# Kernel tuning notes

Measured on AMD Instinct MI355X. Metric: run time of the kernel, lower is better.

## Reference

```python
import jax, jax.numpy as jnp
import numpy as np

B, N, D = 512, 256, 128
N_LAYER, N_HEAD = 4, 1
VAR = 0.01
HEAD = 0  # head_choice in run_mode=0


def setup_inputs() -> dict:
    key = jax.random.key(0)
    k1, k2 = jax.random.split(key)
    Z = jax.random.normal(k1, (B, N + 1, D + 1), dtype=jnp.float32)
    # allparam ~ N(0, var): torch .normal_(0, var) uses var as stddev
    allparam = jax.random.normal(k2, (N_LAYER, N_HEAD, 2, D, D), dtype=jnp.float32) * VAR
    gamma = jnp.ones((N_LAYER, N_HEAD, 1, N + 1, D + 1), dtype=jnp.float32)
    return {"Z": Z, "allparam": allparam, "gamma": gamma}


def _pad_full(M, corner):
    # Embed d x d matrix in (d+1) x (d+1) with zeros; set bottom-right corner.
    d = M.shape[0]
    full = jnp.zeros((d + 1, d + 1), M.dtype).at[:d, :d].set(M)
    return full.at[d, d].set(corner)


def _attention(P, Q, Z):
    # Z: [B, N+1, d+1]
    n = Z.shape[1] - 1
    P_full = _pad_full(P, 1.0)   # P with 1 at [d, d]
    Q_full = _pad_full(Q, 0.0)
    Attn = jnp.einsum('bni,ij,bmj->bnm', Z, Q_full, Z)  # [B, N+1, N+1]
    key = jnp.einsum('ij,bnj->bni', P_full, Z)           # [B, N+1, d+1]
    # A = eye(N+1) with A[N, N] = 0  <=>  zero the last token's key row
    key = key.at[:, n, :].set(0.0)
    return jnp.einsum('bnm,bmi->bni', Attn, key) / n


def reference(Z, allparam, gamma):
    # run_mode=0, chosen head = HEAD
    # T_i = R_i + sum_{k<i} R_k * gamma_k ; Z <- Z + T_i
    acc = jnp.zeros_like(Z)  # running sum_{k<i} R_k * gamma_k
    for i in range(N_LAYER):
        P = allparam[i, HEAD, 0]
        Q = allparam[i, HEAD, 1]
        R = _attention(P, Q, Z)
        T = R + acc
        acc = acc + R * gamma[i, HEAD, 0]
        Z = Z + T
    return Z
```

## Files before the change

### kernel.cpp

```cpp
#include <hip/hip_runtime.h>
#include <hip/hip_bf16.h>
#include <stdint.h>


using short8 = __attribute__((ext_vector_type(8))) short;
using f32x4  = __attribute__((ext_vector_type(4))) float;

#define MFMA16(A,B,C) __builtin_amdgcn_mfma_f32_16x16x32_bf16((A),(B),(C),0,0,0)

static __device__ __forceinline__ uint16_t f2bf(float f){
  union{__hip_bfloat16 h;uint16_t u;}c; c.h=__float2bfloat16(f); return c.u; }
static __device__ __forceinline__ uint32_t pk2(float lo,float hi){
  return (uint32_t)f2bf(lo) | ((uint32_t)f2bf(hi)<<16); }
static __device__ __forceinline__ float bfu(uint16_t u){ return __uint_as_float(((uint32_t)u)<<16); }
static __device__ __forceinline__ float bflo(uint32_t p){ return __uint_as_float(p<<16); }
static __device__ __forceinline__ float bfhi(uint32_t p){ return __uint_as_float(p&0xffff0000u); }

union F4 { uint32_t u[4]; short8 s8; };

#define ZTP   280
#define BUFP  136
#define SCRP  40
#define ZT_OFF   0
#define BUF_OFF  71680
#define SCR_OFF  106496
#define ZBAR_OFF 116736
#define Z256_OFF 117776
#define A128_OFF 118288
#define A256_OFF 119312
#define G_OFF    119840
#define M1_OFF   120352
#define LDS_TOTAL 120864

__global__ __launch_bounds__(512)
__attribute__((amdgpu_waves_per_eu(2, 2)))
void tf_layers(const float* __restrict__ Zin, const float* __restrict__ gamma,
               const uint16_t* __restrict__ Qg, const uint16_t* __restrict__ Pg,
               float* __restrict__ Zout)
{
  extern __shared__ char lds[];
  uint16_t* ZT    = (uint16_t*)(lds + ZT_OFF);
  uint16_t* Gb    = (uint16_t*)(lds + BUF_OFF);
  float*    zbar  = (float*)(lds + ZBAR_OFF);
  float*    z256f = (float*)(lds + Z256_OFF);
  float*    acc128= (float*)(lds + A128_OFF);
  float*    acc256= (float*)(lds + A256_OFF);
  float*    gv    = (float*)(lds + G_OFF);
  float*    m1v   = (float*)(lds + M1_OFF);

  const int tid = threadIdx.x, lane = tid & 63, w = tid >> 6;
  const int l15 = lane & 15, g4 = lane >> 4;
  const int b = blockIdx.x;
  const float inv_n = 1.0f/256.0f;

  uint16_t* scr = (uint16_t*)(lds + SCR_OFF) + w * 16 * SCRP;

  const float* Zb = Zin + (size_t)b*33153;
  float*       Zo = Zout + (size_t)b*33153;

  uint4* accb = (uint4*)(((uintptr_t)Zo + 15) & ~(uintptr_t)15);

  for (int i2 = tid; i2 < 33153; i2 += 512) {
    int r = i2/129, c = i2 - r*129;
    float v = Zb[i2];
    if (c < 128) { ZT[c*ZTP + r] = f2bf(v); if (r == 256) z256f[c] = v; }
    else zbar[r] = v;
  }
  if (tid < 256) acc128[tid] = 0.0f;
  if (tid < 129) acc256[tid] = 0.0f;

  uint32_t lopk[2][16];
#pragma unroll
  for (int ti = 0; ti < 2; ++ti) {
    const int mb = 16*w + 128*ti;
#pragma unroll
    for (int it = 0; it < 8; ++it) {
      const float* zp = Zb + (size_t)(mb + 4*g4)*129 + 16*it + l15;
      float v0 = zp[0], v1 = zp[129], v2 = zp[258], v3 = zp[387];
      lopk[ti][2*it]   = pk2(v0 - bfu(f2bf(v0)), v1 - bfu(f2bf(v1)));
      lopk[ti][2*it+1] = pk2(v2 - bfu(f2bf(v2)), v3 - bfu(f2bf(v3)));
    }
  }

#pragma unroll 1
  for (int l = 0; l < 4; ++l) {
    const uint16_t* Ql  = Qg + l*16384;
    const uint16_t* Pl  = Pg + l*16384;
    const float*    gml = gamma + l*33153;
    const bool last = (l == 3);

    __syncthreads();

    {
      f32x4 gacc[8];
#pragma unroll
      for (int jt = 0; jt < 8; ++jt) gacc[jt] = (f32x4){0,0,0,0};
#pragma unroll
      for (int mw = 0; mw < 8; ++mw) {
        short8 af = *(const short8*)(ZT + (16*w+l15)*ZTP + 32*mw + 8*g4);
#pragma unroll
        for (int jt = 0; jt < 8; ++jt) {
          short8 bf = *(const short8*)(ZT + (16*jt+l15)*ZTP + 32*mw + 8*g4);
          gacc[jt] = MFMA16(af, bf, gacc[jt]);
        }
      }
#pragma unroll
      for (int jt = 0; jt < 8; ++jt)
        *(uint2*)(Gb + (16*jt+l15)*BUFP + 16*w + 4*g4) =
            make_uint2(pk2(gacc[jt][0],gacc[jt][1]), pk2(gacc[jt][2],gacc[jt][3]));
      {
        const int i = tid >> 2, q = lane & 3;
        const uint16_t* zr = ZT + i*ZTP + 64*q;
        float s = 0;
#pragma unroll
        for (int j = 0; j < 16; ++j) {
          uint2 zv = *(const uint2*)(zr + 4*j);
          f32x4 z4 = *(const f32x4*)(zbar + 64*q + 4*j);
          s += bflo(zv.x)*z4[0] + bfhi(zv.x)*z4[1] + bflo(zv.y)*z4[2] + bfhi(zv.y)*z4[3];
        }
        s += __shfl_xor(s,1); s += __shfl_xor(s,2);
        if (q == 0) gv[i] = s;
      }
    }
    __syncthreads();

    uint32_t t1t[16];
    {
      short8 bq[4];
#pragma unroll
      for (int k = 0; k < 4; ++k)
        bq[k] = *(const short8*)(Pl + (16*w+l15)*128 + 32*k + 8*g4);
#pragma unroll
      for (int it = 0; it < 8; ++it) {
        f32x4 d4 = {0,0,0,0};
#pragma unroll
        for (int k = 0; k < 4; ++k) {
          short8 ag = *(const short8*)(Gb + (16*it+l15)*BUFP + 32*k + 8*g4);
          d4 = MFMA16(ag, bq[k], d4);
        }
        t1t[2*it]   = pk2(d4[0], d4[1]);
        t1t[2*it+1] = pk2(d4[2], d4[3]);
      }
      {
        const int d = tid >> 2, q = lane & 3;
        float s = 0;
#pragma unroll
        for (int j = 0; j < 4; ++j) {
          short8 qv = *(const short8*)(Ql + d*128 + 32*q + 8*j);
          f32x4 g0 = *(const f32x4*)(gv + 32*q + 8*j);
          f32x4 g1 = *(const f32x4*)(gv + 32*q + 8*j + 4);
          s += bfu((uint16_t)qv[0])*g0[0] + bfu((uint16_t)qv[1])*g0[1]
             + bfu((uint16_t)qv[2])*g0[2] + bfu((uint16_t)qv[3])*g0[3]
             + bfu((uint16_t)qv[4])*g1[0] + bfu((uint16_t)qv[5])*g1[1]
             + bfu((uint16_t)qv[6])*g1[2] + bfu((uint16_t)qv[7])*g1[3];
        }
        s += __shfl_xor(s,1); s += __shfl_xor(s,2);
        if (q == 0) m1v[d] = s;
      }
    }
    __syncthreads();

    {
      F4 bfr[4];
#pragma unroll
      for (int k2 = 0; k2 < 4; ++k2) {
        *(uint2*)(scr + l15*SCRP + 4*g4)      = make_uint2(t1t[4*k2],   t1t[4*k2+1]);
        *(uint2*)(scr + l15*SCRP + 16 + 4*g4) = make_uint2(t1t[4*k2+2], t1t[4*k2+3]);
        bfr[k2].s8 = *(const short8*)(scr + l15*SCRP + 8*g4);
      }
#pragma unroll
      for (int dt = 0; dt < 8; ++dt) {
        f32x4 d4 = {0,0,0,0};
#pragma unroll
        for (int k2 = 0; k2 < 4; ++k2) {
          short8 aq = *(const short8*)(Ql + (16*dt+l15)*128 + 32*k2 + 8*g4);
          d4 = MFMA16(aq, bfr[k2].s8, d4);
        }
        *(uint2*)(Gb + (16*w+l15)*BUFP + 16*dt + 4*g4) =
            make_uint2(pk2(d4[0],d4[1]), pk2(d4[2],d4[3]));
      }
    }
    __syncthreads();

    float r256v = 0.0f, rcv = 0.0f;
#pragma unroll
    for (int ti = 0; ti < 2; ++ti) {
      const int mb = 16*w + 128*ti;
      F4 aw[4];
      float rp = 0;
#pragma unroll
      for (int q = 0; q < 4; ++q) {
        uint16_t ev[8];
#pragma unroll
        for (int j = 0; j < 8; ++j) ev[j] = ZT[(32*q + 8*g4 + j)*ZTP + mb + l15];
        aw[q].u[0] = (uint32_t)ev[0] | ((uint32_t)ev[1]<<16);
        aw[q].u[1] = (uint32_t)ev[2] | ((uint32_t)ev[3]<<16);
        aw[q].u[2] = (uint32_t)ev[4] | ((uint32_t)ev[5]<<16);
        aw[q].u[3] = (uint32_t)ev[6] | ((uint32_t)ev[7]<<16);
        f32x4 m0 = *(const f32x4*)(m1v + 32*q + 8*g4);
        f32x4 m4 = *(const f32x4*)(m1v + 32*q + 8*g4 + 4);
        rp += bfu(ev[0])*m0[0] + bfu(ev[1])*m0[1] + bfu(ev[2])*m0[2] + bfu(ev[3])*m0[3]
            + bfu(ev[4])*m4[0] + bfu(ev[5])*m4[1] + bfu(ev[6])*m4[2] + bfu(ev[7])*m4[3];
      }
      rp += __shfl_xor(rp,16); rp += __shfl_xor(rp,32);
      rp *= inv_n;
#pragma unroll
      for (int h = 0; h < 2; ++h) {
        f32x4 racc[4];
#pragma unroll
        for (int i = 0; i < 4; ++i) racc[i] = (f32x4){0,0,0,0};
#pragma unroll
        for (int c4 = 0; c4 < 4; ++c4) {
          const int ct = 4*h + c4;
#pragma unroll
          for (int q = 0; q < 4; ++q) {
            short8 bm = *(const short8*)(Gb + (16*ct+l15)*BUFP + 32*q + 8*g4);
            racc[c4] = MFMA16(aw[q].s8, bm, racc[c4]);
          }
        }
        uint32_t ao[8];
        if (l > 0) {
          uint4 q0 = accb[(((ti*2 + h)*2 + 0) << 9) + tid];
          uint4 q1 = accb[(((ti*2 + h)*2 + 1) << 9) + tid];
          ao[0]=q0.x; ao[1]=q0.y; ao[2]=q0.z; ao[3]=q0.w;
          ao[4]=q1.x; ao[5]=q1.y; ao[6]=q1.z; ao[7]=q1.w;
        } else {
#pragma unroll
          for (int i = 0; i < 8; ++i) ao[i] = 0;
        }
        uint32_t an[8];
#pragma unroll
        for (int c4 = 0; c4 < 4; ++c4) {
          const int ct = 4*h + c4;
          uint16_t* zt = ZT + (16*ct+l15)*ZTP + mb + 4*g4;
          uint2 hold = *(uint2*)zt;
          const float* gp = gml + (size_t)(mb + 4*g4)*129 + 16*ct + l15;
          float R0 = racc[c4][0]*inv_n, R1 = racc[c4][1]*inv_n;
          float R2 = racc[c4][2]*inv_n, R3 = racc[c4][3]*inv_n;
          float a0 = bflo(ao[2*c4]),   a1 = bfhi(ao[2*c4]);
          float a2 = bflo(ao[2*c4+1]), a3 = bfhi(ao[2*c4+1]);
          float z0 = bflo(hold.x) + bflo(lopk[ti][2*ct])   + R0 + a0;
          float z1 = bfhi(hold.x) + bfhi(lopk[ti][2*ct])   + R1 + a1;
          float z2 = bflo(hold.y) + bflo(lopk[ti][2*ct+1]) + R2 + a2;
          float z3 = bfhi(hold.y) + bfhi(lopk[ti][2*ct+1]) + R3 + a3;
          an[2*c4]   = pk2(a0 + R0*gp[0],   a1 + R1*gp[129]);
          an[2*c4+1] = pk2(a2 + R2*gp[258], a3 + R3*gp[387]);
          uint16_t h0 = f2bf(z0), h1 = f2bf(z1), h2 = f2bf(z2), h3 = f2bf(z3);
          *(uint2*)zt = make_uint2((uint32_t)h0 | ((uint32_t)h1<<16),
                                   (uint32_t)h2 | ((uint32_t)h3<<16));
          lopk[ti][2*ct]   = pk2(z0 - bfu(h0), z1 - bfu(h1));
          lopk[ti][2*ct+1] = pk2(z2 - bfu(h2), z3 - bfu(h3));
        }
        if (!last) {
          accb[(((ti*2 + h)*2 + 0) << 9) + tid] = make_uint4(an[0],an[1],an[2],an[3]);
          accb[(((ti*2 + h)*2 + 1) << 9) + tid] = make_uint4(an[4],an[5],an[6],an[7]);
        }
      }
      if (lane < 16) {
        const int m = mb + l15;
        float zb = zbar[m], a = acc128[m], ga = gml[m*129 + 128];
        float zn = zb + rp + a;
        zbar[m] = zn; acc128[m] = a + rp*ga;
      }
    }
    {
      const int c = tid >> 2, q = lane & 3;
      float s = 0;
#pragma unroll
      for (int j = 0; j < 8; ++j) {
        const int d0 = 32*q + 4*j;
        uint2 mv = *(const uint2*)(Gb + c*BUFP + d0);
        s += bfu(ZT[d0*ZTP + 256])*bflo(mv.x) + bfu(ZT[(d0+1)*ZTP + 256])*bfhi(mv.x)
           + bfu(ZT[(d0+2)*ZTP + 256])*bflo(mv.y) + bfu(ZT[(d0+3)*ZTP + 256])*bfhi(mv.y);
      }
      s += __shfl_xor(s,1); s += __shfl_xor(s,2);
      r256v = s;
    }
    if (w == 0) {
      const int d0 = lane*2;
      float s = bfu(ZT[d0*ZTP + 256])*m1v[d0] + bfu(ZT[(d0+1)*ZTP + 256])*m1v[d0+1];
      s += __shfl_xor(s,1); s += __shfl_xor(s,2); s += __shfl_xor(s,4);
      s += __shfl_xor(s,8); s += __shfl_xor(s,16); s += __shfl_xor(s,32);
      rcv = s;
    }
    __syncthreads();

    if ((lane & 3) == 0) {
      const int c = tid >> 2;
      float R = r256v*inv_n;
      float z = z256f[c], a = acc256[c], ga = gml[256*129 + c];
      float zn = z + R + a;
      z256f[c] = zn; acc256[c] = a + R*ga; ZT[c*ZTP + 256] = f2bf(zn);
    }
    if (w == 0 && lane == 0) {
      float R = rcv*inv_n;
      float ga = gml[256*129 + 128];
      float zn = zbar[256] + R + acc256[128];
      zbar[256] = zn; acc256[128] = acc256[128] + R*ga;
    }
  }

  __syncthreads();
  for (int i2 = tid; i2 < 33153; i2 += 512) {
    int r = i2/129, c = i2 - r*129;
    float v;
    if (c < 128) v = (r == 256) ? z256f[c] : bfu(ZT[c*ZTP + r]);
    else         v = zbar[r];
    Zo[i2] = v;
  }
}

__global__ void prep_params(const float* __restrict__ ap,
                            uint16_t* __restrict__ qg, uint16_t* __restrict__ pg)
{
  int t = blockIdx.x * 256 + threadIdx.x;
  int l = t >> 14, rem = t & 16383;
  pg[t] = f2bf(ap[(l*2 + 0)*16384 + rem]);
  qg[t] = f2bf(ap[(l*2 + 1)*16384 + rem]);
}

extern "C" void kernel_launch(void* const* d_in, const int* in_sizes, int n_in,
                              void* d_out, int out_size, void* d_ws, size_t ws_size,
                              hipStream_t stream)
{
  const float* Z  = (const float*)d_in[0];
  const float* ap = (const float*)d_in[1];
  const float* gm = (const float*)d_in[2];

  uint16_t* qg = (uint16_t*)d_ws;
  uint16_t* pg = qg + 4*128*128;

  (void)hipFuncSetAttribute((const void*)tf_layers,
                            hipFuncAttributeMaxDynamicSharedMemorySize, LDS_TOTAL);

  prep_params<<<256, 256, 0, stream>>>(ap, qg, pg);
  tf_layers<<<512, 512, LDS_TOTAL, stream>>>(Z, gm, qg, pg, (float*)d_out);
}
```

Baseline: 267.6 us.

## Swizzle ZT layout, double-buffer G scratch, drop a barrier, prefetch accumulators

Replaces the padded ZT row stride with an XOR-swizzled 256-wide layout to cut LDS bank conflicts, and keeps the last token row only in fp32 z256f. Splits the G scratch into two buffers so the barrier between the P and Q GEMM stages can be removed, and loads the accumulator words from global memory before the MFMA loop so their latency overlaps compute. LDS use grows to about 146 KB, and the last-token products now use fp32 values instead of bf16.

```diff
diff --git a/kernel.cpp b/kernel.cpp
--- a/kernel.cpp
+++ b/kernel.cpp
@@ -18,19 +18,23 @@
 
 union F4 { uint32_t u[4]; short8 s8; };
 
-#define ZTP   280
+static __device__ __forceinline__ int ztix(int d, int tok) {
+  return (d << 8) + ((((tok >> 3) ^ (d & 7) ^ ((d >> 3) & 3)) & 31) << 3) + (tok & 7);
+}
+
 #define BUFP  136
 #define SCRP  40
 #define ZT_OFF   0
-#define BUF_OFF  71680
-#define SCR_OFF  106496
-#define ZBAR_OFF 116736
-#define Z256_OFF 117776
-#define A128_OFF 118288
-#define A256_OFF 119312
-#define G_OFF    119840
-#define M1_OFF   120352
-#define LDS_TOTAL 120864
+#define GBA_OFF  65536
+#define GBB_OFF  100352
+#define SCR_OFF  135168
+#define ZBAR_OFF 145408
+#define Z256_OFF 146448
+#define A128_OFF 146960
+#define A256_OFF 147984
+#define G_OFF    148512
+#define M1_OFF   149024
+#define LDS_TOTAL 149536
 
 __global__ __launch_bounds__(512)
 __attribute__((amdgpu_waves_per_eu(2, 2)))
@@ -40,7 +44,8 @@
 {
   extern __shared__ char lds[];
   uint16_t* ZT    = (uint16_t*)(lds + ZT_OFF);
-  uint16_t* Gb    = (uint16_t*)(lds + BUF_OFF);
+  uint16_t* GbA   = (uint16_t*)(lds + GBA_OFF);
+  uint16_t* GbB   = (uint16_t*)(lds + GBB_OFF);
   float*    zbar  = (float*)(lds + ZBAR_OFF);
   float*    z256f = (float*)(lds + Z256_OFF);
   float*    acc128= (float*)(lds + A128_OFF);
@@ -63,7 +68,7 @@
   for (int i2 = tid; i2 < 33153; i2 += 512) {
     int r = i2/129, c = i2 - r*129;
     float v = Zb[i2];
-    if (c < 128) { ZT[c*ZTP + r] = f2bf(v); if (r == 256) z256f[c] = v; }
+    if (c < 128) { if (r < 256) ZT[ztix(c, r)] = f2bf(v); else z256f[c] = v; }
     else zbar[r] = v;
   }
   if (tid < 256) acc128[tid] = 0.0f;
@@ -97,24 +102,23 @@
       for (int jt = 0; jt < 8; ++jt) gacc[jt] = (f32x4){0,0,0,0};
 #pragma unroll
       for (int mw = 0; mw < 8; ++mw) {
-        short8 af = *(const short8*)(ZT + (16*w+l15)*ZTP + 32*mw + 8*g4);
+        short8 af = *(const short8*)(ZT + ztix(16*w + l15, 32*mw + 8*g4));
 #pragma unroll
         for (int jt = 0; jt < 8; ++jt) {
-          short8 bf = *(const short8*)(ZT + (16*jt+l15)*ZTP + 32*mw + 8*g4);
+          short8 bf = *(const short8*)(ZT + ztix(16*jt + l15, 32*mw + 8*g4));
           gacc[jt] = MFMA16(af, bf, gacc[jt]);
         }
       }
 #pragma unroll
       for (int jt = 0; jt < 8; ++jt)
-        *(uint2*)(Gb + (16*jt+l15)*BUFP + 16*w + 4*g4) =
+        *(uint2*)(GbA + (16*jt+l15)*BUFP + 16*w + 4*g4) =
             make_uint2(pk2(gacc[jt][0],gacc[jt][1]), pk2(gacc[jt][2],gacc[jt][3]));
       {
         const int i = tid >> 2, q = lane & 3;
-        const uint16_t* zr = ZT + i*ZTP + 64*q;
         float s = 0;
 #pragma unroll
         for (int j = 0; j < 16; ++j) {
-          uint2 zv = *(const uint2*)(zr + 4*j);
+          uint2 zv = *(const uint2*)(ZT + ztix(i, 64*q + 4*j));
           f32x4 z4 = *(const f32x4*)(zbar + 64*q + 4*j);
           s += bflo(zv.x)*z4[0] + bfhi(zv.x)*z4[1] + bflo(zv.y)*z4[2] + bfhi(zv.y)*z4[3];
         }
@@ -135,7 +139,7 @@
         f32x4 d4 = {0,0,0,0};
 #pragma unroll
         for (int k = 0; k < 4; ++k) {
-          short8 ag = *(const short8*)(Gb + (16*it+l15)*BUFP + 32*k + 8*g4);
+          short8 ag = *(const short8*)(GbA + (16*it+l15)*BUFP + 32*k + 8*g4);
           d4 = MFMA16(ag, bq[k], d4);
         }
         t1t[2*it]   = pk2(d4[0], d4[1]);
@@ -158,7 +162,6 @@
         if (q == 0) m1v[d] = s;
       }
     }
-    __syncthreads();
 
     {
       F4 bfr[4];
@@ -176,7 +179,7 @@
           short8 aq = *(const short8*)(Ql + (16*dt+l15)*128 + 32*k2 + 8*g4);
           d4 = MFMA16(aq, bfr[k2].s8, d4);
         }
-        *(uint2*)(Gb + (16*w+l15)*BUFP + 16*dt + 4*g4) =
+        *(uint2*)(GbB + (16*w+l15)*BUFP + 16*dt + 4*g4) =
             make_uint2(pk2(d4[0],d4[1]), pk2(d4[2],d4[3]));
       }
     }
@@ -186,13 +189,22 @@
 #pragma unroll
     for (int ti = 0; ti < 2; ++ti) {
       const int mb = 16*w + 128*ti;
+      uint4 pf0, pf1, pf2, pf3;
+      if (l > 0) {
+        pf0 = accb[((ti*4 + 0) << 9) + tid];
+        pf1 = accb[((ti*4 + 1) << 9) + tid];
+        pf2 = accb[((ti*4 + 2) << 9) + tid];
+        pf3 = accb[((ti*4 + 3) << 9) + tid];
+      } else {
+        pf0 = pf1 = pf2 = pf3 = make_uint4(0,0,0,0);
+      }
       F4 aw[4];
       float rp = 0;
 #pragma unroll
       for (int q = 0; q < 4; ++q) {
         uint16_t ev[8];
 #pragma unroll
-        for (int j = 0; j < 8; ++j) ev[j] = ZT[(32*q + 8*g4 + j)*ZTP + mb + l15];
+        for (int j = 0; j < 8; ++j) ev[j] = ZT[ztix(32*q + 8*g4 + j, mb + l15)];
         aw[q].u[0] = (uint32_t)ev[0] | ((uint32_t)ev[1]<<16);
         aw[q].u[1] = (uint32_t)ev[2] | ((uint32_t)ev[3]<<16);
         aw[q].u[2] = (uint32_t)ev[4] | ((uint32_t)ev[5]<<16);
@@ -214,25 +226,22 @@
           const int ct = 4*h + c4;
 #pragma unroll
           for (int q = 0; q < 4; ++q) {
-            short8 bm = *(const short8*)(Gb + (16*ct+l15)*BUFP + 32*q + 8*g4);
+            short8 bm = *(const short8*)(GbB + (16*ct+l15)*BUFP + 32*q + 8*g4);
             racc[c4] = MFMA16(aw[q].s8, bm, racc[c4]);
           }
         }
         uint32_t ao[8];
-        if (l > 0) {
-          uint4 q0 = accb[(((ti*2 + h)*2 + 0) << 9) + tid];
-          uint4 q1 = accb[(((ti*2 + h)*2 + 1) << 9) + tid];
+        {
+          uint4 q0 = h ? pf2 : pf0;
+          uint4 q1 = h ? pf3 : pf1;
           ao[0]=q0.x; ao[1]=q0.y; ao[2]=q0.z; ao[3]=q0.w;
           ao[4]=q1.x; ao[5]=q1.y; ao[6]=q1.z; ao[7]=q1.w;
-        } else {
-#pragma unroll
-          for (int i = 0; i < 8; ++i) ao[i] = 0;
         }
         uint32_t an[8];
 #pragma unroll
         for (int c4 = 0; c4 < 4; ++c4) {
           const int ct = 4*h + c4;
-          uint16_t* zt = ZT + (16*ct+l15)*ZTP + mb + 4*g4;
+          uint16_t* zt = ZT + ztix(16*ct + l15, mb + 4*g4);
           uint2 hold = *(uint2*)zt;
           const float* gp = gml + (size_t)(mb + 4*g4)*129 + 16*ct + l15;
           float R0 = racc[c4][0]*inv_n, R1 = racc[c4][1]*inv_n;
@@ -252,8 +261,8 @@
           lopk[ti][2*ct+1] = pk2(z2 - bfu(h2), z3 - bfu(h3));
         }
         if (!last) {
-          accb[(((ti*2 + h)*2 + 0) << 9) + tid] = make_uint4(an[0],an[1],an[2],an[3]);
-          accb[(((ti*2 + h)*2 + 1) << 9) + tid] = make_uint4(an[4],an[5],an[6],an[7]);
+          accb[((ti*4 + h*2 + 0) << 9) + tid] = make_uint4(an[0],an[1],an[2],an[3]);
+          accb[((ti*4 + h*2 + 1) << 9) + tid] = make_uint4(an[4],an[5],an[6],an[7]);
         }
       }
       if (lane < 16) {
@@ -269,16 +278,16 @@
 #pragma unroll
       for (int j = 0; j < 8; ++j) {
         const int d0 = 32*q + 4*j;
-        uint2 mv = *(const uint2*)(Gb + c*BUFP + d0);
-        s += bfu(ZT[d0*ZTP + 256])*bflo(mv.x) + bfu(ZT[(d0+1)*ZTP + 256])*bfhi(mv.x)
-           + bfu(ZT[(d0+2)*ZTP + 256])*bflo(mv.y) + bfu(ZT[(d0+3)*ZTP + 256])*bfhi(mv.y);
+        uint2 mv = *(const uint2*)(GbB + c*BUFP + d0);
+        s += z256f[d0]*bflo(mv.x) + z256f[d0+1]*bfhi(mv.x)
+           + z256f[d0+2]*bflo(mv.y) + z256f[d0+3]*bfhi(mv.y);
       }
       s += __shfl_xor(s,1); s += __shfl_xor(s,2);
       r256v = s;
     }
     if (w == 0) {
       const int d0 = lane*2;
-      float s = bfu(ZT[d0*ZTP + 256])*m1v[d0] + bfu(ZT[(d0+1)*ZTP + 256])*m1v[d0+1];
+      float s = z256f[d0]*m1v[d0] + z256f[d0+1]*m1v[d0+1];
       s += __shfl_xor(s,1); s += __shfl_xor(s,2); s += __shfl_xor(s,4);
       s += __shfl_xor(s,8); s += __shfl_xor(s,16); s += __shfl_xor(s,32);
       rcv = s;
@@ -290,7 +299,7 @@
       float R = r256v*inv_n;
       float z = z256f[c], a = acc256[c], ga = gml[256*129 + c];
       float zn = z + R + a;
-      z256f[c] = zn; acc256[c] = a + R*ga; ZT[c*ZTP + 256] = f2bf(zn);
+      z256f[c] = zn; acc256[c] = a + R*ga;
     }
     if (w == 0 && lane == 0) {
       float R = rcv*inv_n;
@@ -304,7 +313,7 @@
   for (int i2 = tid; i2 < 33153; i2 += 512) {
     int r = i2/129, c = i2 - r*129;
     float v;
-    if (c < 128) v = (r == 256) ? z256f[c] : bfu(ZT[c*ZTP + r]);
+    if (c < 128) v = (r == 256) ? z256f[c] : bfu(ZT[ztix(c, r)]);
     else         v = zbar[r];
     Zo[i2] = v;
   }
```

After: 393.5 us. +47.0%, slower.
